# Performance work log

Hardware: AMD Instinct MI355X
Metric: run time of the kernel (lower is better)

Reference implementation:

```python
import jax, jax.numpy as jnp
import numpy as np

N_NODES = 50000
N_EDGES = 1250000
IN_CH = 64
HID = 64
N_CLASSES = 10
N_GRAPHS = 128


def _xavier(key, shape):
    fan_out, fan_in = shape
    limit = np.sqrt(6.0 / (fan_in + fan_out))
    return jax.random.uniform(key, shape, jnp.float32, -limit, limit)


def setup_inputs() -> dict:
    key = jax.random.key(0)
    ks = jax.random.split(key, 12)
    x = jax.random.normal(ks[0], (N_NODES, IN_CH), jnp.float32)
    edge_index = jax.random.randint(ks[1], (2, N_EDGES), 0, N_NODES, jnp.int64)
    batch = jnp.sort(jax.random.randint(ks[2], (N_NODES,), 0, N_GRAPHS, jnp.int64))
    return {
        "x": x,
        "edge_index": edge_index,
        "batch": batch,
        # GraphConv i: lin_rel (weight+bias) applied to aggregated neighbors,
        # lin_root (no bias) applied to self features. Weights are [out, in].
        "W1_rel": _xavier(ks[3], (HID, IN_CH)), "b1": jnp.zeros((HID,), jnp.float32),
        "W1_root": _xavier(ks[4], (HID, IN_CH)),
        "W2_rel": _xavier(ks[5], (HID, HID)), "b2": jnp.zeros((HID,), jnp.float32),
        "W2_root": _xavier(ks[6], (HID, HID)),
        "W3_rel": _xavier(ks[7], (HID, HID)), "b3": jnp.zeros((HID,), jnp.float32),
        "W3_root": _xavier(ks[8], (HID, HID)),
        "W_lin": _xavier(ks[9], (N_CLASSES, HID)), "b_lin": jnp.zeros((N_CLASSES,), jnp.float32),
    }


def _graph_conv(x, src, dst, W_rel, b, W_root):
    # sum-aggregate neighbor features: gather at src, scatter-add at dst
    agg = jax.ops.segment_sum(x[src], dst, num_segments=N_NODES)  # [N, F]
    return agg @ W_rel.T + b + x @ W_root.T


def reference(x, edge_index, batch, W1_rel, b1, W1_root, W2_rel, b2, W2_root,
              W3_rel, b3, W3_root, W_lin, b_lin):
    src, dst = edge_index[0], edge_index[1]
    h = jax.nn.relu(_graph_conv(x, src, dst, W1_rel, b1, W1_root))
    h = jax.nn.relu(_graph_conv(h, src, dst, W2_rel, b2, W2_root))
    h = _graph_conv(h, src, dst, W3_rel, b3, W3_root)
    # global mean pool over graphs
    sums = jax.ops.segment_sum(h, batch, num_segments=N_GRAPHS)        # [G, HID]
    counts = jax.ops.segment_sum(jnp.ones((h.shape[0],), h.dtype), batch,
                                 num_segments=N_GRAPHS)
    pooled = sums / jnp.maximum(counts, 1.0)[:, None]
    out = pooled @ W_lin.T + b_lin  # dropout inactive in eval mode
    return (pooled, out)
```

## Files before the change

kernel.cpp:

```cpp
#include <hip/hip_runtime.h>

#define N_NODES   50000
#define HID       64
#define N_GRAPHS  128
#define N_CLASSES 10
#define NP        196
#define EPA       8192
#define PCAP      8192

typedef __attribute__((ext_vector_type(8))) short short8;
typedef __attribute__((ext_vector_type(4))) float f32x4;

__device__ __forceinline__ unsigned bf16rne(float f) {
    unsigned u = __float_as_uint(f);
    return (u + 0x7fffu + ((u >> 16) & 1u)) >> 16;
}
__device__ __forceinline__ unsigned pack_bf16x2(float lo, float hi) {
    return bf16rne(lo) | (bf16rne(hi) << 16);
}


__global__ __launch_bounds__(256) void bucket_kernel(
    const int* __restrict__ src, const int* __restrict__ dst,
    int* __restrict__ gcursor, unsigned* __restrict__ packed, int E) {
    __shared__ int hist[NP], scp[NP], base[NP], cnt2[NP];
    __shared__ int sc[256];
    __shared__ unsigned stag[EPA];
    const int t = threadIdx.x;
    const int e0 = blockIdx.x * EPA;
    const int e1 = min(e0 + EPA, E);
    for (int i = t; i < NP; i += 256) { hist[i] = 0; cnt2[i] = 0; }
    __syncthreads();
    for (int e = e0 + t; e < e1; e += 256)
        atomicAdd(&hist[dst[e] >> 8], 1);
    __syncthreads();
    sc[t] = (t < NP) ? hist[t] : 0;
    __syncthreads();
    for (int off = 1; off < 256; off <<= 1) {
        int add = (t >= off) ? sc[t - off] : 0;
        __syncthreads();
        sc[t] += add;
        __syncthreads();
    }
    if (t < NP) {
        scp[t] = sc[t] - hist[t];
        if (hist[t] > 0) base[t] = atomicAdd(&gcursor[t], hist[t]);
    }
    __syncthreads();
    for (int e = e0 + t; e < e1; e += 256) {
        int d = dst[e], s = src[e];
        int p = d >> 8;
        int idx = scp[p] + atomicAdd(&cnt2[p], 1);
        stag[idx] = (unsigned)s | ((unsigned)(d & 255) << 16) | ((unsigned)p << 24);
    }
    __syncthreads();
    const int n = e1 - e0;
    for (int i = t; i < n; i += 256) {
        unsigned v = stag[i];
        int p = v >> 24;
        packed[(size_t)p * PCAP + base[p] + (i - scp[p])] = v & 0x00FFFFFFu;
    }
}

__global__ void pscan_kernel(const int* __restrict__ gcursor,
                             int* __restrict__ pbase, int* __restrict__ offsets) {
    __shared__ int sc[256], v0[256];
    int t = threadIdx.x;
    int v = (t < NP) ? gcursor[t] : 0;
    sc[t] = v; v0[t] = v;
    __syncthreads();
    for (int off = 1; off < 256; off <<= 1) {
        int add = (t >= off) ? sc[t - off] : 0;
        __syncthreads();
        sc[t] += add;
        __syncthreads();
    }
    if (t < NP) pbase[t] = sc[t] - v0[t];
    if (t == 255) { pbase[NP] = sc[255]; offsets[N_NODES] = sc[255]; }
}

__global__ __launch_bounds__(256) void build_kernel(
    const unsigned* __restrict__ packed, const int* __restrict__ pbase,
    int* __restrict__ offsets, unsigned short* __restrict__ csr) {
    __shared__ int hist[256], lofs[256], cnt[256], sc[256];
    __shared__ unsigned short lcsr[PCAP];
    const int p = blockIdx.x, t = threadIdx.x;
    const int pb = pbase[p], ne = pbase[p + 1] - pb;
    const unsigned* mypk = packed + (size_t)p * PCAP;
    hist[t] = 0; cnt[t] = 0;
    __syncthreads();
    for (int i = t; i < ne; i += 256)
        atomicAdd(&hist[(mypk[i] >> 16) & 255], 1);
    __syncthreads();
    sc[t] = hist[t];
    __syncthreads();
    for (int off = 1; off < 256; off <<= 1) {
        int add = (t >= off) ? sc[t - off] : 0;
        __syncthreads();
        sc[t] += add;
        __syncthreads();
    }
    lofs[t] = sc[t] - hist[t];
    int node = p * 256 + t;
    if (node < N_NODES) offsets[node] = pb + lofs[t];
    __syncthreads();
    for (int i = t; i < ne; i += 256) {
        unsigned v = mypk[i];
        int dl = (v >> 16) & 255;
        int slot = lofs[dl] + atomicAdd(&cnt[dl], 1);
        lcsr[slot] = (unsigned short)(v & 0xFFFFu);
    }
    __syncthreads();
    for (int i = t; i < ne; i += 256) csr[pb + i] = lcsr[i];
}


__global__ void cvt_kernel(const float* __restrict__ x, unsigned short* __restrict__ xb, int n4) {
    int i = blockIdx.x * blockDim.x + threadIdx.x;
    if (i < n4) {
        float4 v = ((const float4*)x)[i];
        uint2 o;
        o.x = pack_bf16x2(v.x, v.y);
        o.y = pack_bf16x2(v.z, v.w);
        ((uint2*)xb)[i] = o;
    }
}


__global__ __launch_bounds__(256) void gather_kernel(
    const unsigned short* __restrict__ hin,
    const int* __restrict__ offsets, const unsigned short* __restrict__ csr_src,
    unsigned short* __restrict__ agg) {
    const int w = threadIdx.x >> 6, lane = threadIdx.x & 63;
    const int half = lane >> 5, hl = lane & 31;
    const int n = blockIdx.x * 4 + w;
    const int beg = offsets[n], end = offsets[n + 1];

    float accx = 0.f, accy = 0.f;
    for (int base = beg; base < end; base += 64) {
        int cnt = min(64, end - base);
        int s = (base + lane < end) ? (int)csr_src[base + lane] : 0;
        for (int kb = 0; kb < 64; kb += 16) {
            if (kb >= cnt) break;
            unsigned u[8];
#pragma unroll
            for (int p = 0; p < 8; ++p) {
                int e = kb + 2 * p + half;
                int r = __shfl(s, e);
                u[p] = (e < cnt) ? *((const unsigned*)(hin + (size_t)r * 64) + hl) : 0u;
            }
#pragma unroll
            for (int p = 0; p < 8; ++p) {
                accx += __uint_as_float(u[p] << 16);
                accy += __uint_as_float(u[p] & 0xffff0000u);
            }
        }
    }
    float ox = accx + __shfl(accx, lane ^ 32);
    float oy = accy + __shfl(accy, lane ^ 32);
    if (half == 0)
        *((unsigned*)(agg + (size_t)n * 64) + hl) = pack_bf16x2(ox, oy);
}


template <int RELU>
__global__ __launch_bounds__(256) void linear_kernel(
    const unsigned short* __restrict__ agg,
    const unsigned short* __restrict__ hin,
    const float* __restrict__ Wrel, const float* __restrict__ bias,
    const float* __restrict__ Wroot, unsigned short* __restrict__ hout) {
    __shared__ unsigned short outT[4][16][72];

    const int tid = threadIdx.x;
    const int w = tid >> 6, lane = tid & 63;
    const int q = lane >> 4, c = lane & 15;
    const int g0 = (blockIdx.x * 4 + w) * 16;
    if (g0 >= N_NODES) return;

    short8 brel[4][2], broot[4][2];
    float biasv[4];
#pragma unroll
    for (int t = 0; t < 4; ++t) {
        int o = t * 16 + c;
        biasv[t] = bias[o];
#pragma unroll
        for (int s = 0; s < 2; ++s) {
            const float4* pr = (const float4*)(Wrel  + o * 64 + s * 32 + q * 8);
            const float4* po = (const float4*)(Wroot + o * 64 + s * 32 + q * 8);
            float4 r0 = pr[0], r1 = pr[1], z0 = po[0], z1 = po[1];
            short8 rr, zz;
            rr[0] = (short)bf16rne(r0.x); rr[1] = (short)bf16rne(r0.y);
            rr[2] = (short)bf16rne(r0.z); rr[3] = (short)bf16rne(r0.w);
            rr[4] = (short)bf16rne(r1.x); rr[5] = (short)bf16rne(r1.y);
            rr[6] = (short)bf16rne(r1.z); rr[7] = (short)bf16rne(r1.w);
            zz[0] = (short)bf16rne(z0.x); zz[1] = (short)bf16rne(z0.y);
            zz[2] = (short)bf16rne(z0.z); zz[3] = (short)bf16rne(z0.w);
            zz[4] = (short)bf16rne(z1.x); zz[5] = (short)bf16rne(z1.y);
            zz[6] = (short)bf16rne(z1.z); zz[7] = (short)bf16rne(z1.w);
            brel[t][s] = rr; broot[t][s] = zz;
        }
    }

    const int na = min(g0 + c, N_NODES - 1);
    short8 a_agg[2], a_x[2];
#pragma unroll
    for (int s = 0; s < 2; ++s) {
        a_agg[s] = *(const short8*)(agg + (size_t)na * 64 + s * 32 + q * 8);
        a_x[s]   = *(const short8*)(hin + (size_t)na * 64 + s * 32 + q * 8);
    }

    f32x4 acc4[4];
#pragma unroll
    for (int t = 0; t < 4; ++t) {
        f32x4 a0 = {biasv[t], biasv[t], biasv[t], biasv[t]};
        a0 = __builtin_amdgcn_mfma_f32_16x16x32_bf16(a_agg[0], brel[t][0], a0, 0, 0, 0);
        a0 = __builtin_amdgcn_mfma_f32_16x16x32_bf16(a_agg[1], brel[t][1], a0, 0, 0, 0);
        a0 = __builtin_amdgcn_mfma_f32_16x16x32_bf16(a_x[0],  broot[t][0], a0, 0, 0, 0);
        a0 = __builtin_amdgcn_mfma_f32_16x16x32_bf16(a_x[1],  broot[t][1], a0, 0, 0, 0);
        acc4[t] = a0;
    }

#pragma unroll
    for (int t = 0; t < 4; ++t)
#pragma unroll
        for (int r = 0; r < 4; ++r) {
            float v = acc4[t][r];
            if (RELU) v = fmaxf(v, 0.f);
            outT[w][q * 4 + r][t * 16 + c] = (unsigned short)bf16rne(v);
        }

#pragma unroll
    for (int it = 0; it < 2; ++it) {
        int row = it * 8 + (lane >> 3);
        int ch = (lane & 7) * 8;
        int n = g0 + row;
        if (n < N_NODES) {
            short8 v = *(const short8*)&outT[w][row][ch];
            *(short8*)(hout + (size_t)n * 64 + ch) = v;
        }
    }
}


__global__ __launch_bounds__(256) void pool_kernel(
    const unsigned short* __restrict__ h, const int* __restrict__ batch,
    float* __restrict__ sums, int* __restrict__ cnt) {
    int tid = threadIdx.x;
    int w = tid >> 6, lane = tid & 63;
    int n0 = blockIdx.x * 128 + w * 32;
    if (n0 >= N_NODES) return;
    int nend = min(n0 + 32, N_NODES);
    int cur = batch[n0];
    float acc = 0.f;
    int run = 0;
    for (int n = n0; n < nend; ++n) {
        int g = batch[n];
        if (g != cur) {
            atomicAdd(&sums[cur * 64 + lane], acc);
            if (lane == 0) atomicAdd(&cnt[cur], run);
            acc = 0.f; run = 0; cur = g;
        }
        unsigned u = h[(size_t)n * 64 + lane];
        acc += __uint_as_float(u << 16);
        run++;
    }
    atomicAdd(&sums[cur * 64 + lane], acc);
    if (lane == 0) atomicAdd(&cnt[cur], run);
}

__global__ void final_kernel(const float* __restrict__ sums, const int* __restrict__ cnt,
                             const float* __restrict__ Wlin, const float* __restrict__ blin,
                             float* __restrict__ out) {
    __shared__ float pl[64];
    int g = blockIdx.x, lane = threadIdx.x;
    float cdiv = fmaxf((float)cnt[g], 1.0f);
    float p = sums[g * 64 + lane] / cdiv;
    out[g * 64 + lane] = p;
    pl[lane] = p;
    __syncthreads();
    if (lane < N_CLASSES) {
        float o = blin[lane];
#pragma unroll
        for (int k = 0; k < 64; ++k) o += pl[k] * Wlin[lane * 64 + k];
        out[N_GRAPHS * 64 + g * N_CLASSES + lane] = o;
    }
}


extern "C" void kernel_launch(void* const* d_in, const int* in_sizes, int n_in,
                              void* d_out, int out_size, void* d_ws, size_t ws_size,
                              hipStream_t stream) {
    const float* x     = (const float*)d_in[0];
    const int*   ei    = (const int*)d_in[1];
    const int*   batch = (const int*)d_in[2];
    const float* W1r = (const float*)d_in[3];
    const float* b1  = (const float*)d_in[4];
    const float* W1o = (const float*)d_in[5];
    const float* W2r = (const float*)d_in[6];
    const float* b2  = (const float*)d_in[7];
    const float* W2o = (const float*)d_in[8];
    const float* W3r = (const float*)d_in[9];
    const float* b3  = (const float*)d_in[10];
    const float* W3o = (const float*)d_in[11];
    const float* Wl  = (const float*)d_in[12];
    const float* bl  = (const float*)d_in[13];
    float* out = (float*)d_out;

    const int E = in_sizes[1] / 2;
    const int* src = ei;
    const int* dst = ei + E;

    char* p = (char*)d_ws;
    unsigned short* xb  = (unsigned short*)p; p += (size_t)N_NODES * 64 * 2;
    unsigned short* h1  = (unsigned short*)p; p += (size_t)N_NODES * 64 * 2;
    unsigned short* h2  = (unsigned short*)p; p += (size_t)N_NODES * 64 * 2;
    unsigned short* agg = (unsigned short*)p; p += (size_t)N_NODES * 64 * 2;
    unsigned short* h3  = h1;
    unsigned* packed    = (unsigned*)p; p += (size_t)NP * PCAP * 4;
    unsigned short* csr = (unsigned short*)p; p += (size_t)E * 2;
    int* offsets   = (int*)p;   p += (size_t)(N_NODES + 1) * 4;
    int* gcursor   = (int*)p;   p += NP * 4;
    int* pbase     = (int*)p;   p += (NP + 1) * 4;
    float* sums    = (float*)p; p += (size_t)N_GRAPHS * 64 * 4;
    int* cnt       = (int*)p;   p += N_GRAPHS * 4;

    hipMemsetAsync(gcursor, 0, NP * 4, stream);
    hipMemsetAsync(sums, 0, (size_t)(N_GRAPHS * 64 + N_GRAPHS) * 4, stream);

    const int NCHUNK = (E + EPA - 1) / EPA;
    bucket_kernel<<<NCHUNK, 256, 0, stream>>>(src, dst, gcursor, packed, E);
    cvt_kernel<<<(N_NODES * 64 / 4 + 255) / 256, 256, 0, stream>>>(x, xb, N_NODES * 64 / 4);
    pscan_kernel<<<1, 256, 0, stream>>>(gcursor, pbase, offsets);
    build_kernel<<<NP, 256, 0, stream>>>(packed, pbase, offsets, csr);

    const int GB = N_NODES / 4;
    const int LB = (N_NODES + 63) / 64;
    gather_kernel<<<GB, 256, 0, stream>>>(xb, offsets, csr, agg);
    linear_kernel<1><<<LB, 256, 0, stream>>>(agg, xb, W1r, b1, W1o, h1);
    gather_kernel<<<GB, 256, 0, stream>>>(h1, offsets, csr, agg);
    linear_kernel<1><<<LB, 256, 0, stream>>>(agg, h1, W2r, b2, W2o, h2);
    gather_kernel<<<GB, 256, 0, stream>>>(h2, offsets, csr, agg);
    linear_kernel<0><<<LB, 256, 0, stream>>>(agg, h2, W3r, b3, W3o, h3);

    pool_kernel<<<(N_NODES + 127) / 128, 256, 0, stream>>>(h3, batch, sums, cnt);
    final_kernel<<<N_GRAPHS, 64, 0, stream>>>(sums, cnt, Wl, bl, out);
}
```

Measured before the change: 284.7 us.

## Store node features in 16-channel slabs and gather one slab per block

Node features are stored slab-major: four slabs of 16 bf16 channels, each holding all nodes. The gather kernel's grid now runs slab by slab, so a slab's concurrent working set is much smaller than the full feature table and may stay cache-resident during the random neighbour gathers. Each wave now loads 16 edges per instruction, 8 bytes per lane, and reduces with xor-shuffles. The conversion, linear and pool kernels are updated to read and write the new layout. In exchange, the CSR indices are read four times and each row access shrinks to 32 bytes, which may under-use cache lines.

Result: slower. 367.5 us (+29.1%).

```diff
diff --git a/kernel.cpp b/kernel.cpp
--- a/kernel.cpp
+++ b/kernel.cpp
@@ -7,6 +7,8 @@
 #define NP        196
 #define EPA       8192
 #define PCAP      8192
+#define NSLAB     4
+#define GBLK      12500
 
 typedef __attribute__((ext_vector_type(8))) short short8;
 typedef __attribute__((ext_vector_type(4))) float f32x4;
@@ -18,6 +20,7 @@
 __device__ __forceinline__ unsigned pack_bf16x2(float lo, float hi) {
     return bf16rne(lo) | (bf16rne(hi) << 16);
 }
+
 
 
 __global__ __launch_bounds__(256) void bucket_kernel(
@@ -115,15 +118,15 @@
 }
 
 
-__global__ void cvt_kernel(const float* __restrict__ x, unsigned short* __restrict__ xb, int n4) {
-    int i = blockIdx.x * blockDim.x + threadIdx.x;
-    if (i < n4) {
-        float4 v = ((const float4*)x)[i];
-        uint2 o;
-        o.x = pack_bf16x2(v.x, v.y);
-        o.y = pack_bf16x2(v.z, v.w);
-        ((uint2*)xb)[i] = o;
-    }
+__global__ void cvt_kernel(const float* __restrict__ x, unsigned short* __restrict__ xb) {
+    int tid = blockIdx.x * blockDim.x + threadIdx.x;
+    if (tid >= N_NODES * 16) return;
+    int n = tid >> 4, r = tid & 15, s = r >> 2, cp = r & 3;
+    float4 v = *(const float4*)(x + (size_t)n * 64 + r * 4);
+    uint2 o;
+    o.x = pack_bf16x2(v.x, v.y);
+    o.y = pack_bf16x2(v.z, v.w);
+    *(uint2*)(xb + ((size_t)s * N_NODES + n) * 16 + cp * 4) = o;
 }
 
 
@@ -132,34 +135,45 @@
     const int* __restrict__ offsets, const unsigned short* __restrict__ csr_src,
     unsigned short* __restrict__ agg) {
     const int w = threadIdx.x >> 6, lane = threadIdx.x & 63;
-    const int half = lane >> 5, hl = lane & 31;
-    const int n = blockIdx.x * 4 + w;
+    const int s  = blockIdx.x / GBLK;
+    const int nb = blockIdx.x % GBLK;
+    const int n = nb * 4 + w;
+    const int rg = lane >> 2, cp = lane & 3;
     const int beg = offsets[n], end = offsets[n + 1];
-
-    float accx = 0.f, accy = 0.f;
+    const unsigned short* hs = hin + (size_t)s * N_NODES * 16;
+
+    float a0 = 0.f, a1 = 0.f, a2 = 0.f, a3 = 0.f;
     for (int base = beg; base < end; base += 64) {
         int cnt = min(64, end - base);
-        int s = (base + lane < end) ? (int)csr_src[base + lane] : 0;
-        for (int kb = 0; kb < 64; kb += 16) {
-            if (kb >= cnt) break;
-            unsigned u[8];
-#pragma unroll
-            for (int p = 0; p < 8; ++p) {
-                int e = kb + 2 * p + half;
-                int r = __shfl(s, e);
-                u[p] = (e < cnt) ? *((const unsigned*)(hin + (size_t)r * 64) + hl) : 0u;
-            }
-#pragma unroll
-            for (int p = 0; p < 8; ++p) {
-                accx += __uint_as_float(u[p] << 16);
-                accy += __uint_as_float(u[p] & 0xffff0000u);
-            }
-        }
-    }
-    float ox = accx + __shfl(accx, lane ^ 32);
-    float oy = accy + __shfl(accy, lane ^ 32);
-    if (half == 0)
-        *((unsigned*)(agg + (size_t)n * 64) + hl) = pack_bf16x2(ox, oy);
+        int sidx = (base + lane < end) ? (int)csr_src[base + lane] : 0;
+        uint2 u[4] = {{0u,0u},{0u,0u},{0u,0u},{0u,0u}};
+#pragma unroll
+        for (int p = 0; p < 4; ++p) {
+            int e = p * 16 + rg;
+            int r = __shfl(sidx, e);
+            if (e < cnt) u[p] = *(const uint2*)(hs + (size_t)r * 16 + cp * 4);
+        }
+#pragma unroll
+        for (int p = 0; p < 4; ++p) {
+            a0 += __uint_as_float(u[p].x << 16);
+            a1 += __uint_as_float(u[p].x & 0xffff0000u);
+            a2 += __uint_as_float(u[p].y << 16);
+            a3 += __uint_as_float(u[p].y & 0xffff0000u);
+        }
+    }
+#pragma unroll
+    for (int m = 4; m <= 32; m <<= 1) {
+        a0 += __shfl_xor(a0, m);
+        a1 += __shfl_xor(a1, m);
+        a2 += __shfl_xor(a2, m);
+        a3 += __shfl_xor(a3, m);
+    }
+    if (lane < 4) {
+        uint2 o;
+        o.x = pack_bf16x2(a0, a1);
+        o.y = pack_bf16x2(a2, a3);
+        *(uint2*)(agg + ((size_t)s * N_NODES + n) * 16 + lane * 4) = o;
+    }
 }
 
 
@@ -205,8 +219,10 @@
     short8 a_agg[2], a_x[2];
 #pragma unroll
     for (int s = 0; s < 2; ++s) {
-        a_agg[s] = *(const short8*)(agg + (size_t)na * 64 + s * 32 + q * 8);
-        a_x[s]   = *(const short8*)(hin + (size_t)na * 64 + s * 32 + q * 8);
+        int ss = s * 2 + (q >> 1);
+        size_t off = ((size_t)ss * N_NODES + na) * 16 + (q & 1) * 8;
+        a_agg[s] = *(const short8*)(agg + off);
+        a_x[s]   = *(const short8*)(hin + off);
     }
 
     f32x4 acc4[4];
@@ -229,14 +245,13 @@
             outT[w][q * 4 + r][t * 16 + c] = (unsigned short)bf16rne(v);
         }
 
-#pragma unroll
-    for (int it = 0; it < 2; ++it) {
-        int row = it * 8 + (lane >> 3);
-        int ch = (lane & 7) * 8;
-        int n = g0 + row;
-        if (n < N_NODES) {
-            short8 v = *(const short8*)&outT[w][row][ch];
-            *(short8*)(hout + (size_t)n * 64 + ch) = v;
+    const int row = lane >> 2, cp = lane & 3;
+    const int n2 = g0 + row;
+#pragma unroll
+    for (int s = 0; s < 4; ++s) {
+        if (n2 < N_NODES) {
+            uint2 v = *(const uint2*)&outT[w][row][s * 16 + cp * 4];
+            *(uint2*)(hout + ((size_t)s * N_NODES + n2) * 16 + cp * 4) = v;
         }
     }
 }
@@ -250,6 +265,8 @@
     int n0 = blockIdx.x * 128 + w * 32;
     if (n0 >= N_NODES) return;
     int nend = min(n0 + 32, N_NODES);
+    const unsigned short* hs = h + (size_t)(lane >> 4) * N_NODES * 16;
+    int c16 = lane & 15;
     int cur = batch[n0];
     float acc = 0.f;
     int run = 0;
@@ -260,7 +277,7 @@
             if (lane == 0) atomicAdd(&cnt[cur], run);
             acc = 0.f; run = 0; cur = g;
         }
-        unsigned u = h[(size_t)n * 64 + lane];
+        unsigned u = hs[(size_t)n * 16 + c16];
         acc += __uint_as_float(u << 16);
         run++;
     }
@@ -329,11 +346,11 @@
 
     const int NCHUNK = (E + EPA - 1) / EPA;
     bucket_kernel<<<NCHUNK, 256, 0, stream>>>(src, dst, gcursor, packed, E);
-    cvt_kernel<<<(N_NODES * 64 / 4 + 255) / 256, 256, 0, stream>>>(x, xb, N_NODES * 64 / 4);
+    cvt_kernel<<<(N_NODES * 16 + 255) / 256, 256, 0, stream>>>(x, xb);
     pscan_kernel<<<1, 256, 0, stream>>>(gcursor, pbase, offsets);
     build_kernel<<<NP, 256, 0, stream>>>(packed, pbase, offsets, csr);
 
-    const int GB = N_NODES / 4;
+    const int GB = NSLAB * GBLK;
     const int LB = (N_NODES + 63) / 64;
     gather_kernel<<<GB, 256, 0, stream>>>(xb, offsets, csr, agg);
     linear_kernel<1><<<LB, 256, 0, stream>>>(agg, xb, W1r, b1, W1o, h1);
```
